# Performance work log

Measured on AMD Instinct MI355X. Metric: run time of the kernel, lower is better.

Reference implementation:

```python
import jax, jax.numpy as jnp
import numpy as np

HEADS = 8

def _conv1d(x, w, b, pad, groups):
    # x: (B, C_in, T), w: (C_out, C_in/groups, K)
    out = jax.lax.conv_general_dilated(
        x, w, window_strides=(1,), padding=[(pad, pad)],
        feature_group_count=groups,
        dimension_numbers=('NCH', 'OIH', 'NCH'))
    if b is not None:
        out = out + b[None, :, None]
    return out


def setup_inputs() -> dict:
    key = jax.random.key(0)
    ks = jax.random.split(key, 9)
    B, T, D, H = 8, 4096, 512, HEADS
    s = 0.02
    return {
        'x': jax.random.normal(ks[0], (B, T, D), jnp.float32),
        'W_qkv': jax.random.normal(ks[1], (D, 3 * D), jnp.float32) * s,
        'w_qkv_dw': jax.random.normal(ks[2], (3 * D, 1, 3), jnp.float32) * s,
        'w_ctx1': jax.random.normal(ks[3], (D, 1, 3), jnp.float32) * s,
        'w_ctx2': jax.random.normal(ks[4], (D, 1, 5), jnp.float32) * s,
        'W_fc': jax.random.normal(ks[5], (3 * H, 9), jnp.float32) * s,
        'b_fc': jnp.zeros((9,), jnp.float32),
        'w_dep': jax.random.normal(ks[6], (D, 9, 3), jnp.float32) * s,
        'b_dep': jnp.zeros((D,), jnp.float32),
        'temperature': jnp.ones((H, 1, 1), jnp.float32),
    }


def reference(x, W_qkv, w_qkv_dw, w_ctx1, w_ctx2, W_fc, b_fc, w_dep, b_dep, temperature):
    B, T, D = x.shape
    H = HEADS
    C = D // H  # channels per head

    # qkv linear + depthwise conv (k=3)
    qkv = x @ W_qkv                                       # (B,T,3D)
    qkv = _conv1d(qkv.transpose(0, 2, 1), w_qkv_dw, None, 1, 3 * D).transpose(0, 2, 1)

    # fc branch: (B,T,3H,C) -> fc over the 3H axis -> (B,T,9,C)
    f_all = qkv.reshape(B, T, 3 * H, C)
    f = jnp.einsum('bthc,hn->btnc', f_all, W_fc) + b_fc[None, None, :, None]
    f_conv = f.reshape(B, T, 9 * C).transpose(0, 2, 1)    # (B, 9C, T)
    out_conv = _conv1d(f_conv, w_dep, b_dep, 1, C).transpose(0, 2, 1)  # (B,T,D)

    # channel attention: q,k,v -> (B,H,C,T), L2-normalize over T
    q, k, v = jnp.split(qkv, 3, axis=-1)
    def to_heads(z):
        return z.reshape(B, T, H, C).transpose(0, 2, 3, 1)  # (B,H,C,T)
    q, k, v = to_heads(q), to_heads(k), to_heads(v)
    q = q / jnp.maximum(jnp.linalg.norm(q, axis=-1, keepdims=True), 1e-12)
    k = k / jnp.maximum(jnp.linalg.norm(k, axis=-1, keepdims=True), 1e-12)
    attn = jnp.einsum('bhct,bhdt->bhcd', q, k) * temperature  # (B,H,C,C)
    attn = jax.nn.softmax(attn, axis=-1)
    out_att = jnp.einsum('bhcd,bhdt->bhct', attn, v)
    out_att = out_att.transpose(0, 3, 1, 2).reshape(B, T, D)

    # regional context: depthwise k=3 -> ReLU -> depthwise k=5
    ctx = _conv1d(x.transpose(0, 2, 1), w_ctx1, None, 1, D)
    ctx = jax.nn.relu(ctx)
    ctx = _conv1d(ctx, w_ctx2, None, 2, D).transpose(0, 2, 1)

    return ctx + out_conv + out_att
```

## Files before the change

kernel.cpp:

```cpp
#include <hip/hip_runtime.h>

typedef __attribute__((ext_vector_type(8))) _Float16 f16x8;
typedef __attribute__((ext_vector_type(4))) _Float16 f16x4;
typedef __attribute__((ext_vector_type(4))) float f32x4;

__device__ inline void gl_lds16(const void* g, void* l) {
  __builtin_amdgcn_global_load_lds(
      (const __attribute__((address_space(1))) unsigned int*)g,
      (__attribute__((address_space(3))) unsigned int*)l, 16, 0, 0);
}

__global__ __launch_bounds__(256) void zero_k(float* __restrict__ g, float* __restrict__ n) {
  int i = (blockIdx.x << 8) + threadIdx.x;
  if (i < 262144) g[i] = 0.f;
  if (i < 12288) n[i] = 0.f;
}

__global__ __launch_bounds__(256) void split_x_k(
    const float* __restrict__ x, _Float16* __restrict__ hi) {
  int i = (blockIdx.x << 8) + threadIdx.x;
  float4 v = ((const float4*)x)[i];
  f16x4 h;
  h[0] = (_Float16)v.x; h[1] = (_Float16)v.y;
  h[2] = (_Float16)v.z; h[3] = (_Float16)v.w;
  *(f16x4*)&hi[(size_t)i << 2] = h;
}

__global__ __launch_bounds__(256) void split_wt_k(
    const float* __restrict__ w, _Float16* __restrict__ hi) {
  __shared__ float tile[32][33];
  int k0 = blockIdx.x << 5;
  int n0 = blockIdx.y << 5;
  int r = threadIdx.x >> 5, c = threadIdx.x & 31;
#pragma unroll
  for (int i = 0; i < 4; ++i)
    tile[r + (i << 3)][c] = w[(size_t)(k0 + r + (i << 3)) * 1536 + n0 + c];
  __syncthreads();
#pragma unroll
  for (int i = 0; i < 4; ++i) {
    int n = r + (i << 3), k = c;
    hi[(size_t)(n0 + n) * 512 + k0 + k] = (_Float16)tile[k][n];
  }
}

__global__ __launch_bounds__(256) void gemm_qkv_k(
    const _Float16* __restrict__ xhi, const _Float16* __restrict__ whi,
    _Float16* __restrict__ qkv) {
  __shared__ _Float16 As[3][128 * 32];
  __shared__ _Float16 Bs[3][128 * 32];
  const int tid = threadIdx.x;
  const int wave = tid >> 6, lane = tid & 63;
  const int orig = blockIdx.x;
  const int wg = ((orig & 7) * 384) + (orig >> 3);
  const int bm = wg / 12;
  const int bn = wg - bm * 12;
  const int wm = (wave >> 1) << 6, wn = (wave & 1) << 6;
  const int lhi = lane >> 4, llo = lane & 15;

  f32x4 zero = {};
  f32x4 acc[4][4];
#pragma unroll
  for (int i = 0; i < 4; ++i)
#pragma unroll
    for (int j = 0; j < 4; ++j) acc[i][j] = zero;

  const int srowA = (bm << 7) + (wave << 5) + (lane >> 2);
  const int srowB = (bn << 7) + (wave << 5) + (lane >> 2);
  const int kc = (((lane & 3) ^ ((lane >> 3) & 3)) << 3);
  const size_t aoff0 = ((size_t)srowA << 9) + kc;
  const size_t aoff1 = ((size_t)(srowA + 16) << 9) + kc;
  const size_t boff0 = ((size_t)srowB << 9) + kc;
  const size_t boff1 = ((size_t)(srowB + 16) << 9) + kc;
  const int wb0 = (wave << 5) << 5;
  const int wb1 = ((wave << 5) + 16) << 5;

  auto stage = [&](int buf, int kk) {
    const int k0 = kk << 5;
    gl_lds16(xhi + aoff0 + k0, &As[buf][wb0]);
    gl_lds16(xhi + aoff1 + k0, &As[buf][wb1]);
    gl_lds16(whi + boff0 + k0, &Bs[buf][wb0]);
    gl_lds16(whi + boff1 + k0, &Bs[buf][wb1]);
  };

  stage(0, 0);
  stage(1, 1);
  int cur = 0;
  for (int kk = 0; kk < 16; ++kk) {
    if (kk < 14) {
      stage((cur + 2) % 3, kk + 2);
      asm volatile("s_waitcnt vmcnt(8)" ::: "memory");
    } else if (kk == 14) {
      asm volatile("s_waitcnt vmcnt(4)" ::: "memory");
    } else {
      asm volatile("s_waitcnt vmcnt(0)" ::: "memory");
    }
    __builtin_amdgcn_s_barrier();
    __builtin_amdgcn_sched_barrier(0);
    const int ksw = ((lhi ^ ((llo >> 1) & 3)) << 3);
    f16x8 af[4], bf[4];
#pragma unroll
    for (int mi = 0; mi < 4; ++mi)
      af[mi] = *(const f16x8*)&As[cur][((wm + (mi << 4) + llo) << 5) + ksw];
#pragma unroll
    for (int ni = 0; ni < 4; ++ni)
      bf[ni] = *(const f16x8*)&Bs[cur][((wn + (ni << 4) + llo) << 5) + ksw];
    __builtin_amdgcn_s_setprio(1);
#pragma unroll
    for (int mi = 0; mi < 4; ++mi)
#pragma unroll
      for (int ni = 0; ni < 4; ++ni)
        acc[mi][ni] = __builtin_amdgcn_mfma_f32_16x16x32_f16(af[mi], bf[ni], acc[mi][ni], 0, 0, 0);
    __builtin_amdgcn_s_setprio(0);
    __builtin_amdgcn_sched_barrier(0);
    __builtin_amdgcn_s_barrier();
    cur = (cur + 1) % 3;
  }
#pragma unroll
  for (int mi = 0; mi < 4; ++mi) {
    const int row0 = (bm << 7) + wm + (mi << 4) + (lhi << 2);
#pragma unroll
    for (int ni = 0; ni < 4; ++ni) {
      const int col = (bn << 7) + wn + (ni << 4) + llo;
      _Float16* p = qkv + (size_t)row0 * 1536 + col;
#pragma unroll
      for (int r = 0; r < 4; ++r) p[(size_t)r * 1536] = (_Float16)acc[mi][ni][r];
    }
  }
}

__global__ __launch_bounds__(192) void dwconv_k(
    const _Float16* __restrict__ qkv, const float* __restrict__ w3,
    _Float16* __restrict__ qkvc, float* __restrict__ partials) {
  int g = threadIdx.x;
  int c0 = g << 3;
  int bt = blockIdx.x;
  int b = bt >> 6;
  int t0 = (bt & 63) << 6;
  const _Float16* base = qkv + ((size_t)((b << 12) + t0)) * 1536 + c0;
  _Float16* obase = qkvc + ((size_t)((b << 12) + t0)) * 1536 + c0;
  float w0[8], w1[8], w2[8];
#pragma unroll
  for (int j = 0; j < 8; ++j) {
    w0[j] = w3[(c0 + j) * 3 + 0];
    w1[j] = w3[(c0 + j) * 3 + 1];
    w2[j] = w3[(c0 + j) * 3 + 2];
  }
  f16x8 zero8 = {};
  f16x8 pv = (t0 == 0) ? zero8 : *(const f16x8*)&base[-1536];
  f16x8 cv = *(const f16x8*)&base[0];
  float ss[8] = {};
  for (int i = 0; i < 64; ++i) {
    f16x8 nv = (t0 + i == 4095) ? zero8 : *(const f16x8*)&base[(size_t)(i + 1) * 1536];
    f16x8 o;
#pragma unroll
    for (int j = 0; j < 8; ++j) {
      float of = (float)pv[j] * w0[j] + (float)cv[j] * w1[j] + (float)nv[j] * w2[j];
      _Float16 oh = (_Float16)of;
      o[j] = oh;
      float orf = (float)oh;
      ss[j] += orf * orf;
    }
    *(f16x8*)&obase[(size_t)i * 1536] = o;
    pv = cv; cv = nv;
  }
  float* pp = partials + ((size_t)(bt & 63)) * 12288 + b * 1536 + c0;
  *(float4*)pp = make_float4(ss[0], ss[1], ss[2], ss[3]);
  *(float4*)(pp + 4) = make_float4(ss[4], ss[5], ss[6], ss[7]);
}

__global__ __launch_bounds__(256) void reduce_norms_k(
    const float* __restrict__ partials, float* __restrict__ norms) {
  int i = (blockIdx.x << 8) + threadIdx.x;
  float s = 0.f;
  for (int ch = 0; ch < 64; ++ch) s += partials[(size_t)ch * 12288 + i];
  norms[i] = s;
}

__global__ __launch_bounds__(256) void attn_gram_k(
    const _Float16* __restrict__ qkvc, float* __restrict__ Gbuf) {
  int bh = blockIdx.x;  int b = bh >> 3, h = bh & 7;
  int tq = blockIdx.y;
  __shared__ float qb[64][68];
  __shared__ float kb[64][68];
  float acc[4][4] = {};
  int cr = threadIdx.x >> 4, dc = threadIdx.x & 15;
  int coff = h << 6;
  for (int ch = 0; ch < 4; ++ch) {
    int tb = (tq << 8) + (ch << 6);
    __syncthreads();
#pragma unroll
    for (int i = 0; i < 2; ++i) {
      int idx = (i << 8) + threadIdx.x;
      int tl = idx >> 3, g8 = (idx & 7) << 3;
      const _Float16* gp = qkvc + ((size_t)((b << 12) + tb + tl)) * 1536 + coff + g8;
      f16x8 qv8 = *(const f16x8*)gp;
      f16x8 kv8 = *(const f16x8*)(gp + 512);
      float* qd = &qb[tl][g8];
      float* kd = &kb[tl][g8];
#pragma unroll
      for (int j = 0; j < 8; ++j) { qd[j] = (float)qv8[j]; kd[j] = (float)kv8[j]; }
    }
    __syncthreads();
#pragma unroll 8
    for (int tl = 0; tl < 64; ++tl) {
      float4 qv = *(const float4*)&qb[tl][cr << 2];
      float4 kv = *(const float4*)&kb[tl][dc << 2];
      float qa[4] = {qv.x, qv.y, qv.z, qv.w};
      float ka[4] = {kv.x, kv.y, kv.z, kv.w};
#pragma unroll
      for (int i = 0; i < 4; ++i)
#pragma unroll
        for (int j = 0; j < 4; ++j) acc[i][j] += qa[i] * ka[j];
    }
  }
  float* Gp = Gbuf + ((size_t)bh << 12);
#pragma unroll
  for (int i = 0; i < 4; ++i)
#pragma unroll
    for (int j = 0; j < 4; ++j)
      atomicAdd(&Gp[((cr << 2) + i) * 64 + (dc << 2) + j], acc[i][j]);
}

__global__ __launch_bounds__(256) void attn_softmax_k(
    const float* __restrict__ Gbuf, const float* __restrict__ norms,
    const float* __restrict__ temp, float* __restrict__ attn) {
  int tid = threadIdx.x;
  int sub = tid >> 6, c = tid & 63;
  int bh = (blockIdx.x << 2) + sub;
  int b = bh >> 3, h = bh & 7;
  __shared__ float nk[4][64];
  float nq = fmaxf(sqrtf(norms[b * 1536 + (h << 6) + c]), 1e-12f);
  nk[sub][c] = fmaxf(sqrtf(norms[b * 1536 + 512 + (h << 6) + c]), 1e-12f);
  __syncthreads();
  float inq = temp[h] / nq;
  const float* Gp = Gbuf + ((size_t)bh << 12) + c * 64;
  float mx = -3.0e38f;
  for (int d = 0; d < 64; ++d) mx = fmaxf(mx, Gp[d] / nk[sub][d] * inq);
  float s = 0.f;
  for (int d = 0; d < 64; ++d) s += expf(Gp[d] / nk[sub][d] * inq - mx);
  float inv = 1.0f / s;
  float* op = attn + ((size_t)bh << 12) + c * 64;
  for (int d = 0; d < 64; ++d) op[d] = expf(Gp[d] / nk[sub][d] * inq - mx) * inv;
}

__global__ __launch_bounds__(256) void attn_out_k(
    const _Float16* __restrict__ qkvc, const float* __restrict__ attn,
    float* __restrict__ out) {
  int blk = blockIdx.x;
  int tt = blk & 31, h = (blk >> 5) & 7, b = blk >> 8;
  int t0 = tt << 7;
  __shared__ float atT[64][68];
  __shared__ float vbT[64][132];
  int tid = threadIdx.x;
  const float* ap = attn + ((size_t)((b << 3) + h) << 12);
#pragma unroll
  for (int i = 0; i < 16; ++i) {
    int idx = (i << 8) + tid;  int c2 = idx >> 6, e = idx & 63;
    atT[e][c2] = ap[idx];
  }
#pragma unroll
  for (int i = 0; i < 32; ++i) {
    int idx = (i << 8) + tid;  int t = idx >> 6, e = idx & 63;
    vbT[e][t] = (float)qkvc[((size_t)((b << 12) + t0 + t)) * 1536 + 1024 + (h << 6) + e];
  }
  __syncthreads();
  int tg = tid >> 4, cg = tid & 15;
  float acc[8][4] = {};
#pragma unroll 2
  for (int e = 0; e < 64; ++e) {
    float4 av = *(const float4*)&atT[e][cg << 2];
    float4 v0 = *(const float4*)&vbT[e][tg << 3];
    float4 v1 = *(const float4*)&vbT[e][(tg << 3) + 4];
    float va[8] = {v0.x, v0.y, v0.z, v0.w, v1.x, v1.y, v1.z, v1.w};
    float aa[4] = {av.x, av.y, av.z, av.w};
#pragma unroll
    for (int j = 0; j < 8; ++j)
#pragma unroll
      for (int i = 0; i < 4; ++i) acc[j][i] += va[j] * aa[i];
  }
#pragma unroll
  for (int j = 0; j < 8; ++j) {
    int t = t0 + (tg << 3) + j;
    float4 st = make_float4(acc[j][0], acc[j][1], acc[j][2], acc[j][3]);
    *(float4*)&out[(((size_t)((b << 12) + t)) << 9) + (h << 6) + (cg << 2)] = st;
  }
}

__global__ __launch_bounds__(256) void conv2_k(
    const _Float16* __restrict__ qkvc, const float* __restrict__ x,
    const float* __restrict__ wfc, const float* __restrict__ bfc,
    const float* __restrict__ wdep, const float* __restrict__ bdep,
    const float* __restrict__ w1, const float* __restrict__ w2,
    float* __restrict__ out) {
  __shared__ _Float16 fs[18][576];
  __shared__ _Float16 c1[20][512];
  __shared__ float wfcs[216];
  __shared__ float bfcs[9];
  int b = blockIdx.x >> 8;
  int t0 = (blockIdx.x & 255) << 4;
  int tid = threadIdx.x;
  if (tid < 216) wfcs[tid] = wfc[tid];
  else if (tid < 225) bfcs[tid - 216] = bfc[tid - 216];

#pragma unroll
  for (int half = 0; half < 2; ++half) {
    int d = (half << 8) + tid;
    float w10 = w1[d * 3], w11 = w1[d * 3 + 1], w12 = w1[d * 3 + 2];
    const float* xb = x + ((size_t)(b << 12)) * 512 + d;
    int tp0 = t0 - 2;
    float xm = (tp0 - 1 >= 0) ? xb[(size_t)(tp0 - 1) * 512] : 0.f;
    float xc = (tp0 >= 0 && tp0 < 4096) ? xb[(size_t)tp0 * 512] : 0.f;
    for (int tl = 0; tl < 20; ++tl) {
      int tp = tp0 + tl;
      float xp = (tp + 1 >= 0 && tp + 1 < 4096) ? xb[(size_t)(tp + 1) * 512] : 0.f;
      float v = 0.f;
      if (tp >= 0 && tp < 4096)
        v = fmaxf(xm * w10 + xc * w11 + xp * w12, 0.f);
      c1[tl][d] = (_Float16)v;
      xm = xc; xc = xp;
    }
  }
  __syncthreads();

  if (tid < 144) {
    int row = tid / 8, cg = tid & 7;
    int t = t0 - 1 + row;
    int cbase = cg << 3;
    if (t >= 0 && t < 4096) {
      const _Float16* q = qkvc + ((size_t)((b << 12) + t)) * 1536 + cbase;
      float acc9[9][8];
#pragma unroll
      for (int n = 0; n < 9; ++n) {
        float bv = bfcs[n];
#pragma unroll
        for (int j = 0; j < 8; ++j) acc9[n][j] = bv;
      }
      for (int m = 0; m < 24; ++m) {
        f16x8 v = *(const f16x8*)&q[m << 6];
        float vf[8];
#pragma unroll
        for (int j = 0; j < 8; ++j) vf[j] = (float)v[j];
#pragma unroll
        for (int n = 0; n < 9; ++n) {
          float w = wfcs[m * 9 + n];
#pragma unroll
          for (int j = 0; j < 8; ++j) acc9[n][j] += w * vf[j];
        }
      }
#pragma unroll
      for (int n = 0; n < 9; ++n) {
        f16x8 o;
#pragma unroll
        for (int j = 0; j < 8; ++j) o[j] = (_Float16)acc9[n][j];
        *(f16x8*)&fs[row][(n << 6) + cbase] = o;
      }
    } else {
      f16x8 z = {};
#pragma unroll
      for (int n = 0; n < 9; ++n) *(f16x8*)&fs[row][(n << 6) + cbase] = z;
    }
  }
  __syncthreads();

#pragma unroll
  for (int pass = 0; pass < 2; ++pass) {
    int o = (pass << 8) + tid;
    int g9 = (o >> 3) * 9;
    float wd[27];
#pragma unroll
    for (int q = 0; q < 27; ++q) wd[q] = wdep[o * 27 + q];
    float w2r[5];
#pragma unroll
    for (int p = 0; p < 5; ++p) w2r[p] = w2[o * 5 + p];
    float bd = bdep[o];
    float f0[9], f1[9], f2[9];
#pragma unroll
    for (int i = 0; i < 9; ++i) {
      f0[i] = (float)fs[0][g9 + i];
      f1[i] = (float)fs[1][g9 + i];
    }
    float c0 = (float)c1[0][o], cA = (float)c1[1][o], cB = (float)c1[2][o], cC = (float)c1[3][o];
    float* ob = out + ((size_t)((b << 12) + t0)) * 512 + o;
    for (int tl = 0; tl < 16; ++tl) {
      float s = bd;
#pragma unroll
      for (int i = 0; i < 9; ++i) f2[i] = (float)fs[tl + 2][g9 + i];
      float c4 = (float)c1[tl + 4][o];
#pragma unroll
      for (int i = 0; i < 9; ++i)
        s += f0[i] * wd[i * 3 + 0] + f1[i] * wd[i * 3 + 1] + f2[i] * wd[i * 3 + 2];
      s += c0 * w2r[0] + cA * w2r[1] + cB * w2r[2] + cC * w2r[3] + c4 * w2r[4];
      ob[(size_t)tl * 512] += s;
#pragma unroll
      for (int i = 0; i < 9; ++i) { f0[i] = f1[i]; f1[i] = f2[i]; }
      c0 = cA; cA = cB; cB = cC; cC = c4;
    }
  }
}

extern "C" void kernel_launch(void* const* d_in, const int* in_sizes, int n_in,
                              void* d_out, int out_size, void* d_ws, size_t ws_size,
                              hipStream_t stream) {
  (void)in_sizes; (void)n_in; (void)out_size; (void)ws_size;
  const float* x        = (const float*)d_in[0];
  const float* W_qkv    = (const float*)d_in[1];
  const float* w_qkv_dw = (const float*)d_in[2];
  const float* w_ctx1   = (const float*)d_in[3];
  const float* w_ctx2   = (const float*)d_in[4];
  const float* W_fc     = (const float*)d_in[5];
  const float* b_fc     = (const float*)d_in[6];
  const float* w_dep    = (const float*)d_in[7];
  const float* b_dep    = (const float*)d_in[8];
  const float* temperature = (const float*)d_in[9];
  float* out = (float*)d_out;

  char* ws = (char*)d_ws;
  _Float16* xhi  = (_Float16*)(ws);
  _Float16* whi  = (_Float16*)(ws + 100663296);
  float* partials = (float*)(ws + 100663296);
  _Float16* qkv16  = (_Float16*)(ws + 103809024);
  _Float16* qkvc16 = (_Float16*)(ws);
  char* tail = ws + 204472320;
  float* Gbuf  = (float*)(tail);
  float* attn  = (float*)(tail + 1048576);
  float* norms = (float*)(tail + 2097152);

  zero_k<<<1024, 256, 0, stream>>>(Gbuf, norms);
  split_x_k<<<16384, 256, 0, stream>>>(x, xhi);
  split_wt_k<<<dim3(16, 48), 256, 0, stream>>>(W_qkv, whi);
  gemm_qkv_k<<<3072, 256, 0, stream>>>(xhi, whi, qkv16);
  dwconv_k<<<512, 192, 0, stream>>>(qkv16, w_qkv_dw, qkvc16, partials);
  reduce_norms_k<<<48, 256, 0, stream>>>(partials, norms);
  attn_gram_k<<<dim3(64, 16), 256, 0, stream>>>(qkvc16, Gbuf);
  attn_softmax_k<<<16, 256, 0, stream>>>(Gbuf, norms, temperature, attn);
  attn_out_k<<<2048, 256, 0, stream>>>(qkvc16, attn, out);
  conv2_k<<<2048, 256, 0, stream>>>(qkvc16, x, W_fc, b_fc, w_dep, b_dep,
                                    w_ctx1, w_ctx2, out);
}
```

Measured before the change: 365.3 us.

## Stream ctx conv into output loop and vectorize V tile loads

In conv2_k the first depthwise conv plus ReLU is no longer staged through a shared-memory c1 buffer. Each thread now computes its own channel's values in registers inside the output loop. This removes a syncthreads-separated phase and about 20KB of LDS per block, which may raise occupancy. In attn_out_k the V tile load now uses 8-wide f16 vector loads instead of scalar half loads, at the cost of strided LDS transposed writes.

Result: no change. 363.8 us (-0.4%).

```diff
diff --git a/kernel.cpp b/kernel.cpp
--- a/kernel.cpp
+++ b/kernel.cpp
@@ -135,7 +135,8 @@
   int c0 = g << 3;
   int bt = blockIdx.x;
   int b = bt >> 6;
-  int t0 = (bt & 63) << 6;
+  int chunk = bt & 63;
+  int t0 = chunk << 6;
   const _Float16* base = qkv + ((size_t)((b << 12) + t0)) * 1536 + c0;
   _Float16* obase = qkvc + ((size_t)((b << 12) + t0)) * 1536 + c0;
   float w0[8], w1[8], w2[8];
@@ -163,7 +164,7 @@
     *(f16x8*)&obase[(size_t)i * 1536] = o;
     pv = cv; cv = nv;
   }
-  float* pp = partials + ((size_t)(bt & 63)) * 12288 + b * 1536 + c0;
+  float* pp = partials + ((size_t)chunk) * 12288 + b * 1536 + c0;
   *(float4*)pp = make_float4(ss[0], ss[1], ss[2], ss[3]);
   *(float4*)(pp + 4) = make_float4(ss[4], ss[5], ss[6], ss[7]);
 }
@@ -259,9 +260,12 @@
     atT[e][c2] = ap[idx];
   }
 #pragma unroll
-  for (int i = 0; i < 32; ++i) {
-    int idx = (i << 8) + tid;  int t = idx >> 6, e = idx & 63;
-    vbT[e][t] = (float)qkvc[((size_t)((b << 12) + t0 + t)) * 1536 + 1024 + (h << 6) + e];
+  for (int i = 0; i < 4; ++i) {
+    int idx = (i << 8) + tid;
+    int t = idx >> 3, e8 = (idx & 7) << 3;
+    f16x8 v = *(const f16x8*)&qkvc[((size_t)((b << 12) + t0 + t)) * 1536 + 1024 + (h << 6) + e8];
+#pragma unroll
+    for (int j = 0; j < 8; ++j) vbT[e8 + j][t] = (float)v[j];
   }
   __syncthreads();
   int tg = tid >> 4, cg = tid & 15;
@@ -293,7 +297,6 @@
     const float* __restrict__ w1, const float* __restrict__ w2,
     float* __restrict__ out) {
   __shared__ _Float16 fs[18][576];
-  __shared__ _Float16 c1[20][512];
   __shared__ float wfcs[216];
   __shared__ float bfcs[9];
   int b = blockIdx.x >> 8;
@@ -301,25 +304,6 @@
   int tid = threadIdx.x;
   if (tid < 216) wfcs[tid] = wfc[tid];
   else if (tid < 225) bfcs[tid - 216] = bfc[tid - 216];
-
-#pragma unroll
-  for (int half = 0; half < 2; ++half) {
-    int d = (half << 8) + tid;
-    float w10 = w1[d * 3], w11 = w1[d * 3 + 1], w12 = w1[d * 3 + 2];
-    const float* xb = x + ((size_t)(b << 12)) * 512 + d;
-    int tp0 = t0 - 2;
-    float xm = (tp0 - 1 >= 0) ? xb[(size_t)(tp0 - 1) * 512] : 0.f;
-    float xc = (tp0 >= 0 && tp0 < 4096) ? xb[(size_t)tp0 * 512] : 0.f;
-    for (int tl = 0; tl < 20; ++tl) {
-      int tp = tp0 + tl;
-      float xp = (tp + 1 >= 0 && tp + 1 < 4096) ? xb[(size_t)(tp + 1) * 512] : 0.f;
-      float v = 0.f;
-      if (tp >= 0 && tp < 4096)
-        v = fmaxf(xm * w10 + xc * w11 + xp * w12, 0.f);
-      c1[tl][d] = (_Float16)v;
-      xm = xc; xc = xp;
-    }
-  }
   __syncthreads();
 
   if (tid < 144) {
@@ -373,19 +357,43 @@
 #pragma unroll
     for (int p = 0; p < 5; ++p) w2r[p] = w2[o * 5 + p];
     float bd = bdep[o];
+    float w10 = w1[o * 3], w11 = w1[o * 3 + 1], w12 = w1[o * 3 + 2];
+    const float* xb = x + ((size_t)(b << 12)) * 512 + o;
+
+    int tp0 = t0 - 2;
+    float xm = (tp0 - 1 >= 0) ? xb[(size_t)(tp0 - 1) * 512] : 0.f;
+    float xc = (tp0 >= 0 && tp0 < 4096) ? xb[(size_t)tp0 * 512] : 0.f;
+    float cv4[4];
+#pragma unroll
+    for (int i = 0; i < 4; ++i) {
+      int tp = tp0 + i;
+      float xp = (tp + 1 >= 0 && tp + 1 < 4096) ? xb[(size_t)(tp + 1) * 512] : 0.f;
+      float v = 0.f;
+      if (tp >= 0 && tp < 4096)
+        v = fmaxf(xm * w10 + xc * w11 + xp * w12, 0.f);
+      cv4[i] = (float)(_Float16)v;
+      xm = xc; xc = xp;
+    }
+    float c0 = cv4[0], cA = cv4[1], cB = cv4[2], cC = cv4[3];
+
     float f0[9], f1[9], f2[9];
 #pragma unroll
     for (int i = 0; i < 9; ++i) {
       f0[i] = (float)fs[0][g9 + i];
       f1[i] = (float)fs[1][g9 + i];
     }
-    float c0 = (float)c1[0][o], cA = (float)c1[1][o], cB = (float)c1[2][o], cC = (float)c1[3][o];
     float* ob = out + ((size_t)((b << 12) + t0)) * 512 + o;
     for (int tl = 0; tl < 16; ++tl) {
+      int tp = t0 + 2 + tl;
+      float xp = (tp + 1 < 4096) ? xb[(size_t)(tp + 1) * 512] : 0.f;
+      float v4 = 0.f;
+      if (tp < 4096) v4 = fmaxf(xm * w10 + xc * w11 + xp * w12, 0.f);
+      float c4 = (float)(_Float16)v4;
+      xm = xc; xc = xp;
+
       float s = bd;
 #pragma unroll
       for (int i = 0; i < 9; ++i) f2[i] = (float)fs[tl + 2][g9 + i];
-      float c4 = (float)c1[tl + 4][o];
 #pragma unroll
       for (int i = 0; i < 9; ++i)
         s += f0[i] * wd[i * 3 + 0] + f1[i] * wd[i * 3 + 1] + f2[i] * wd[i * 3 + 2];
```
